# Performance work log

Hardware: AMD Instinct MI355X
Metric: run time of the kernel (lower is better)

The kernel has to match this reference:

```python
import jax, jax.numpy as jnp
import numpy as np

NUM_HEADS = 16


def setup_inputs() -> dict:
    key = jax.random.key(0)
    ks = jax.random.split(key, 6)
    B, N, L, C = 2, 1024, 4096, 1024
    x_obj = jax.random.normal(ks[0], (B, N, C), dtype=jnp.float32)
    x_ctx = jax.random.normal(ks[1], (B, L, C), dtype=jnp.float32)
    s = 1.0 / np.sqrt(C)
    Wq = jax.random.normal(ks[2], (C, C), dtype=jnp.float32) * s
    Wkv = jax.random.normal(ks[3], (C, 2 * C), dtype=jnp.float32) * s
    Wproj = jax.random.normal(ks[4], (C, C), dtype=jnp.float32) * s
    bproj = jax.random.normal(ks[5], (C,), dtype=jnp.float32) * 0.01
    return {"x_obj": x_obj, "x_ctx": x_ctx, "Wq": Wq, "Wkv": Wkv,
            "Wproj": Wproj, "bproj": bproj}


def _split_heads(t, H):
    # [B, T, C] -> [B, H, T, d]
    B, T, C = t.shape
    return t.reshape(B, T, H, C // H).transpose(0, 2, 1, 3)


def reference(x_obj, x_ctx, Wq, Wkv, Wproj, bproj):
    B, N, C = x_obj.shape
    H = NUM_HEADS
    d = C // H
    scale = d ** -0.5

    q = _split_heads(x_obj @ Wq, H)                      # [B,H,N,d]

    kv_o = x_obj @ Wkv                                   # [B,N,2C] -> (2,H,d) split
    k_obj = _split_heads(kv_o[..., :C], H)               # [B,H,N,d]
    v_obj = _split_heads(kv_o[..., C:], H)

    kv_c = x_ctx @ Wkv                                   # [B,L,2C]
    k_ctx = _split_heads(kv_c[..., :C], H)               # [B,H,L,d]
    v_ctx = _split_heads(kv_c[..., C:], H)

    k = jnp.concatenate([k_obj, k_ctx], axis=2)          # [B,H,N+L,d]
    v = jnp.concatenate([v_obj, v_ctx], axis=2)

    attn = jnp.einsum('bhnd,bhmd->bhnm', q, k) * scale   # [B,H,N,N+L]
    attn = jax.nn.softmax(attn, axis=-1)
    out = jnp.einsum('bhnm,bhmd->bhnd', attn, v)         # [B,H,N,d]
    out = out.transpose(0, 2, 1, 3).reshape(B, N, C)
    return out @ Wproj + bproj
```

## Files before the change

kernel.cpp:

```cpp
#include <hip/hip_runtime.h>
#include <stdint.h>

typedef unsigned short u16;
typedef unsigned int   u32;
typedef __attribute__((ext_vector_type(8))) short bf16x8;
typedef __attribute__((ext_vector_type(4))) float f32x4;

__device__ __forceinline__ u16 f2bf(float f) {
    union { float f; u32 u; } v; v.f = f;
    return (u16)((v.u + 0x7FFFu + ((v.u >> 16) & 1u)) >> 16);
}
__device__ __forceinline__ float bf2f(u16 h) {
    union { u32 u; float f; } v; v.u = ((u32)h) << 16; return v.f;
}

__device__ __forceinline__ void async16(const u16* g, u16* l) {
    typedef __attribute__((address_space(1))) const u32 gq;
    typedef __attribute__((address_space(3))) u32 lq;
    __builtin_amdgcn_global_load_lds((gq*)g, (lq*)l, 16, 0, 0);
}

__global__ void cvt_cat_k(const float* __restrict__ xo, const float* __restrict__ xc,
                          u16* __restrict__ Xc)
{
    int t = blockIdx.x * 256 + threadIdx.x;
    int row = t >> 8, cid = (t & 255) * 4;
    int b = row >= 5120, s = row - b * 5120;
    const float* src = (s < 1024)
        ? xo + ((size_t)(b * 1024 + s)) * 1024 + cid
        : xc + ((size_t)(b * 4096 + s - 1024)) * 1024 + cid;
    float4 f = *(const float4*)src;
    union { u16 a[4]; uint2 v; } p;
    p.a[0] = f2bf(f.x); p.a[1] = f2bf(f.y); p.a[2] = f2bf(f.z); p.a[3] = f2bf(f.w);
    *(uint2*)(Xc + (size_t)row * 1024 + cid) = p.v;
}

__global__ void cvt_w_k(const float* __restrict__ Wq, const float* __restrict__ Wkv,
                        const float* __restrict__ Wp,
                        u16* __restrict__ Wqt, u16* __restrict__ Wkt,
                        u16* __restrict__ Wpt)
{
    __shared__ __align__(16) u16 Ts[64][72];
    int id = blockIdx.x;
    const float* W; u16* Wt; int N, tile;
    if (id < 256)      { W = Wq;  Wt = Wqt; N = 1024; tile = id; }
    else if (id < 768) { W = Wkv; Wt = Wkt; N = 2048; tile = id - 256; }
    else               { W = Wp;  Wt = Wpt; N = 1024; tile = id - 768; }
    int nt = N >> 6;
    int n0 = (tile % nt) * 64, k0 = (tile / nt) * 64;

    int t = threadIdx.x;
    int lr = t >> 2, lc = (t & 3) * 16;
    const float* src = W + (size_t)(k0 + lr) * N + n0 + lc;
    union { u16 a[8]; uint4 v; } p0, p1;
    float4 f0 = *(const float4*)(src),      f1 = *(const float4*)(src + 4);
    float4 f2 = *(const float4*)(src + 8),  f3 = *(const float4*)(src + 12);
    p0.a[0]=f2bf(f0.x); p0.a[1]=f2bf(f0.y); p0.a[2]=f2bf(f0.z); p0.a[3]=f2bf(f0.w);
    p0.a[4]=f2bf(f1.x); p0.a[5]=f2bf(f1.y); p0.a[6]=f2bf(f1.z); p0.a[7]=f2bf(f1.w);
    p1.a[0]=f2bf(f2.x); p1.a[1]=f2bf(f2.y); p1.a[2]=f2bf(f2.z); p1.a[3]=f2bf(f2.w);
    p1.a[4]=f2bf(f3.x); p1.a[5]=f2bf(f3.y); p1.a[6]=f2bf(f3.z); p1.a[7]=f2bf(f3.w);
    *(uint4*)&Ts[lr][lc]     = p0.v;
    *(uint4*)&Ts[lr][lc + 8] = p1.v;
    __syncthreads();
    union { u16 a[8]; uint4 v; } q0, q1;
#pragma unroll
    for (int j = 0; j < 8; ++j) q0.a[j] = Ts[lc + j][lr];
#pragma unroll
    for (int j = 0; j < 8; ++j) q1.a[j] = Ts[lc + 8 + j][lr];
    u16* dst = Wt + (size_t)(n0 + lr) * 1024 + k0 + lc;
    *(uint4*)dst       = q0.v;
    *(uint4*)(dst + 8) = q1.v;
}

__global__ __launch_bounds__(256, 2)
void gemm_qkv(const u16* __restrict__ A, const u16* __restrict__ Wqt,
              const u16* __restrict__ Wkt, u16* __restrict__ q,
              u16* __restrict__ Kh, u16* __restrict__ Vh)
{
    __shared__ __align__(16) u16 smem[17408];
    u16* As = smem;
    u16* Bs = smem + 4096;

    const int t = threadIdx.x, w = t >> 6;
    const int lane = t & 63, quad = lane >> 4, l16 = lane & 15;
    const int id = blockIdx.x;
    const bool qm = id >= 1280;
    int m0, n0; const u16* Bt;
    if (qm) { int t2 = id - 1280; m0 = (t2 >> 3) * 128; n0 = (t2 & 7) * 128; Bt = Wqt; }
    else    { m0 = (id >> 4) * 128; n0 = (id & 15) * 128; Bt = Wkt; }
    const int wr = (w >> 1) * 64, wc = (w & 1) * 64;

    const int sr0 = w * 32 + (lane >> 2), sr1 = sr0 + 16;
    const int cg  = (lane & 3) ^ ((lane >> 4) & 3);
    u16* abase = As + w * 1024;
    u16* bbase = Bs + w * 1024;

    const u16 *ar0, *ar1;
    {
        int g0 = m0 + sr0, g1 = m0 + sr1;
        if (qm) {
            ar0 = A + ((size_t)(g0 >> 10) * 5120 + (g0 & 1023)) * 1024;
            ar1 = A + ((size_t)(g1 >> 10) * 5120 + (g1 & 1023)) * 1024;
        } else {
            ar0 = A + (size_t)g0 * 1024;
            ar1 = A + (size_t)g1 * 1024;
        }
        ar0 += cg * 8; ar1 += cg * 8;
    }
    const u16* br0 = Bt + (size_t)(n0 + sr0) * 1024 + cg * 8;
    const u16* br1 = Bt + (size_t)(n0 + sr1) * 1024 + cg * 8;

    f32x4 acc[4][4] = {};
    const int sel = (quad ^ (l16 >> 2)) * 8;

    for (int k0 = 0; k0 < 1024; k0 += 32) {
        async16(ar0 + k0, abase);
        async16(ar1 + k0, abase + 512);
        async16(br0 + k0, bbase);
        async16(br1 + k0, bbase + 512);
        __syncthreads();

        bf16x8 av[4], bv[4];
#pragma unroll
        for (int i = 0; i < 4; ++i)
            av[i] = *(const bf16x8*)&As[(wr + i * 16 + l16) * 32 + sel];
#pragma unroll
        for (int j = 0; j < 4; ++j)
            bv[j] = *(const bf16x8*)&Bs[(wc + j * 16 + l16) * 32 + sel];
#pragma unroll
        for (int i = 0; i < 4; ++i)
#pragma unroll
            for (int j = 0; j < 4; ++j)
                acc[i][j] = __builtin_amdgcn_mfma_f32_16x16x32_bf16(av[i], bv[j], acc[i][j], 0, 0, 0);
        __syncthreads();
    }

    if (qm) {
#pragma unroll
        for (int j = 0; j < 4; ++j) {
            int col = n0 + wc + j * 16 + l16;
#pragma unroll
            for (int i = 0; i < 4; ++i) {
                int rowb = m0 + wr + i * 16 + quad * 4;
#pragma unroll
                for (int r = 0; r < 4; ++r)
                    q[(size_t)(rowb + r) * 1024 + col] = f2bf(acc[i][j][r]);
            }
        }
    } else if (n0 < 1024) {
#pragma unroll
        for (int j = 0; j < 4; ++j) {
            int col = n0 + wc + j * 16 + l16;
#pragma unroll
            for (int i = 0; i < 4; ++i) {
                int rowb = m0 + wr + i * 16 + quad * 4;
                int b = rowb >= 5120;
                int key = rowb - b * 5120;
                int bh = b * 16 + (col >> 6), d = col & 63;
                u16* dst = Kh + ((size_t)bh * 5120 + key) * 64 + d;
#pragma unroll
                for (int r = 0; r < 4; ++r) dst[r * 64] = f2bf(acc[i][j][r]);
            }
        }
    } else {
        u16* Tv = smem;
#pragma unroll
        for (int j = 0; j < 4; ++j) {
            int d2 = wc + j * 16 + l16;
#pragma unroll
            for (int i = 0; i < 4; ++i) {
                int kl = wr + i * 16 + quad * 4;
                union { u16 a[4]; uint2 v; } pk;
#pragma unroll
                for (int r = 0; r < 4; ++r) pk.a[r] = f2bf(acc[i][j][r]);
                *(uint2*)&Tv[d2 * 136 + kl] = pk.v;
            }
        }
        __syncthreads();
        int b = m0 >= 5120;
        int keyb = m0 - b * 5120;
        int hb = (n0 - 1024) >> 6;
#pragma unroll
        for (int p = 0; p < 8; ++p) {
            int idx = p * 256 + t;
            int d2 = idx >> 4, k0c = (idx & 15) * 8;
            uint4 vv = *(const uint4*)&Tv[d2 * 136 + k0c];
            int bh = b * 16 + hb + (d2 >> 6), d = d2 & 63;
            *(uint4*)(Vh + ((size_t)bh * 64 + d) * 5120 + keyb + k0c) = vv;
        }
    }
}

__global__ __launch_bounds__(256, 2)
void gemm_proj(const u16* __restrict__ A, const u16* __restrict__ Bt,
               const float* __restrict__ bias, float* __restrict__ Cf)
{
    __shared__ __align__(16) u16 As[128 * 32];
    __shared__ __align__(16) u16 Bs[64 * 32];

    const int t = threadIdx.x, w = t >> 6;
    const int lane = t & 63, quad = lane >> 4, l16 = lane & 15;
    const int m0 = blockIdx.y * 128, n0 = blockIdx.x * 64;
    const int wr = w * 32, wc = 0;

    const int sr0 = w * 32 + (lane >> 2), sr1 = sr0 + 16;
    const int cg  = (lane & 3) ^ ((lane >> 4) & 3);
    u16* abase = As + w * 1024;
    u16* bbase = Bs + w * 512;

    const u16* ar0 = A + (size_t)(m0 + sr0) * 1024 + cg * 8;
    const u16* ar1 = A + (size_t)(m0 + sr1) * 1024 + cg * 8;
    const u16* br0 = Bt + (size_t)(n0 + w * 16 + (lane >> 2)) * 1024 + cg * 8;

    f32x4 acc[2][4] = {};
    const int sel = (quad ^ (l16 >> 2)) * 8;

    for (int k0 = 0; k0 < 1024; k0 += 32) {
        async16(ar0 + k0, abase);
        async16(ar1 + k0, abase + 512);
        async16(br0 + k0, bbase);
        __syncthreads();

        bf16x8 av[2], bv[4];
#pragma unroll
        for (int i = 0; i < 2; ++i)
            av[i] = *(const bf16x8*)&As[(wr + i * 16 + l16) * 32 + sel];
#pragma unroll
        for (int j = 0; j < 4; ++j)
            bv[j] = *(const bf16x8*)&Bs[(wc + j * 16 + l16) * 32 + sel];
#pragma unroll
        for (int i = 0; i < 2; ++i)
#pragma unroll
            for (int j = 0; j < 4; ++j)
                acc[i][j] = __builtin_amdgcn_mfma_f32_16x16x32_bf16(av[i], bv[j], acc[i][j], 0, 0, 0);
        __syncthreads();
    }

#pragma unroll
    for (int j = 0; j < 4; ++j) {
        int col = n0 + wc + j * 16 + l16;
        float bvl = bias[col];
#pragma unroll
        for (int i = 0; i < 2; ++i) {
            int rowb = m0 + wr + i * 16 + quad * 4;
#pragma unroll
            for (int r = 0; r < 4; ++r)
                Cf[(size_t)(rowb + r) * 1024 + col] = acc[i][j][r] + bvl;
        }
    }
}

__global__ __launch_bounds__(256, 4)
void attn_k(const u16* __restrict__ Q, const u16* __restrict__ Kh,
            const u16* __restrict__ Vh, u16* __restrict__ Op,
            float* __restrict__ Lp)
{
    __shared__ __align__(16) u16 Ks[64][72];
    __shared__ __align__(16) u16 Vt[64][72];
    __shared__ __align__(16) u16 Ps[4][32][72];

    const int tid  = threadIdx.x;
    const int wave = tid >> 6, lane = tid & 63;
    const int quad = lane >> 4, l16 = lane & 15;
    const int bx = blockIdx.x;
    const int part = bx & 3, qt = (bx >> 2) & 7, h = (bx >> 5) & 15, b = bx >> 9;
    const int bh = b * 16 + h;

    const int qrow0 = b * 1024 + qt * 128 + wave * 32;
    const u16* qbase = Q + (size_t)qrow0 * 1024 + h * 64;

    bf16x8 aq[2][2];
#pragma unroll
    for (int rt = 0; rt < 2; ++rt) {
        aq[rt][0] = *(const bf16x8*)(qbase + (size_t)(rt * 16 + l16) * 1024 +      quad * 8);
        aq[rt][1] = *(const bf16x8*)(qbase + (size_t)(rt * 16 + l16) * 1024 + 32 + quad * 8);
    }

    f32x4 o[2][4] = {};
    f32x4 lv[2] = {};

    const u16* kbase = Kh + (size_t)bh * 5120 * 64;
    const u16* vbase = Vh + (size_t)bh * 64 * 5120;
    const int skey = tid >> 2, sdc = (tid & 3) * 16;
    const int m_beg = part * 1280;

    for (int c = 0; c < 20; ++c) {
        const int m0 = m_beg + c * 64;
        {
            const u16* src = kbase + (size_t)(m0 + skey) * 64 + sdc;
            *(uint4*)&Ks[skey][sdc]     = *(const uint4*)(src);
            *(uint4*)&Ks[skey][sdc + 8] = *(const uint4*)(src + 8);
        }
        {
            const u16* vsrc = vbase + (size_t)skey * 5120 + m0 + sdc;
            *(uint4*)&Vt[skey][sdc]     = *(const uint4*)(vsrc);
            *(uint4*)&Vt[skey][sdc + 8] = *(const uint4*)(vsrc + 8);
        }
        __syncthreads();

        f32x4 s[2][4] = {};
#pragma unroll
        for (int nt = 0; nt < 4; ++nt) {
            bf16x8 kb0 = *(const bf16x8*)&Ks[nt * 16 + l16][     quad * 8];
            bf16x8 kb1 = *(const bf16x8*)&Ks[nt * 16 + l16][32 + quad * 8];
#pragma unroll
            for (int rt = 0; rt < 2; ++rt) {
                s[rt][nt] = __builtin_amdgcn_mfma_f32_16x16x32_bf16(aq[rt][0], kb0, s[rt][nt], 0, 0, 0);
                s[rt][nt] = __builtin_amdgcn_mfma_f32_16x16x32_bf16(aq[rt][1], kb1, s[rt][nt], 0, 0, 0);
            }
        }

#pragma unroll
        for (int rt = 0; rt < 2; ++rt)
#pragma unroll
            for (int nt = 0; nt < 4; ++nt)
#pragma unroll
                for (int r = 0; r < 4; ++r) {
                    float e = __expf(s[rt][nt][r] * 0.125f);
                    lv[rt][r] += e;
                    Ps[wave][rt * 16 + quad * 4 + r][nt * 16 + l16] = f2bf(e);
                }

        asm volatile("s_waitcnt lgkmcnt(0)" ::: "memory");

        bf16x8 pf[2][2];
#pragma unroll
        for (int rt = 0; rt < 2; ++rt) {
            pf[rt][0] = *(const bf16x8*)&Ps[wave][rt * 16 + l16][     quad * 8];
            pf[rt][1] = *(const bf16x8*)&Ps[wave][rt * 16 + l16][32 + quad * 8];
        }

#pragma unroll
        for (int dt = 0; dt < 4; ++dt) {
            bf16x8 v0 = *(const bf16x8*)&Vt[dt * 16 + l16][     quad * 8];
            bf16x8 v1 = *(const bf16x8*)&Vt[dt * 16 + l16][32 + quad * 8];
#pragma unroll
            for (int rt = 0; rt < 2; ++rt) {
                o[rt][dt] = __builtin_amdgcn_mfma_f32_16x16x32_bf16(pf[rt][0], v0, o[rt][dt], 0, 0, 0);
                o[rt][dt] = __builtin_amdgcn_mfma_f32_16x16x32_bf16(pf[rt][1], v1, o[rt][dt], 0, 0, 0);
            }
        }
        __syncthreads();
    }

    float lsum[2][4];
#pragma unroll
    for (int rt = 0; rt < 2; ++rt)
#pragma unroll
        for (int r = 0; r < 4; ++r) {
            float x = lv[rt][r];
#pragma unroll
            for (int off = 8; off >= 1; off >>= 1)
                x += __shfl_xor(x, off, 64);
            lsum[rt][r] = x;
        }

    const int Rb = bh * 1024 + qt * 128 + wave * 32;
    u16* obase = Op + ((size_t)part << 21);
#pragma unroll
    for (int rt = 0; rt < 2; ++rt)
#pragma unroll
        for (int dt = 0; dt < 4; ++dt)
#pragma unroll
            for (int r = 0; r < 4; ++r) {
                int R = Rb + rt * 16 + quad * 4 + r;
                obase[(size_t)R * 64 + dt * 16 + l16] = f2bf(o[rt][dt][r]);
            }
    if (l16 == 0) {
#pragma unroll
        for (int rt = 0; rt < 2; ++rt)
#pragma unroll
            for (int r = 0; r < 4; ++r)
                Lp[part * 32768 + Rb + rt * 16 + quad * 4 + r] = lsum[rt][r];
    }
}

__global__ void comb_k(const u16* __restrict__ Op, const float* __restrict__ Lp,
                       u16* __restrict__ ao)
{
    int t = blockIdx.x * 256 + threadIdx.x;
    int R = t >> 4, dg = (t & 15) * 4;
    float l = Lp[R] + Lp[32768 + R] + Lp[65536 + R] + Lp[98304 + R];
    float a[4] = {0.f, 0.f, 0.f, 0.f};
#pragma unroll
    for (int p = 0; p < 4; ++p) {
        union { u16 a[4]; uint2 v; } w;
        w.v = *(const uint2*)(Op + ((size_t)p << 21) + (size_t)R * 64 + dg);
#pragma unroll
        for (int j = 0; j < 4; ++j) a[j] += bf2f(w.a[j]);
    }
    float inv = 1.f / l;
    int bh = R >> 10, n = R & 1023, b = bh >> 4, h = bh & 15;
    union { u16 a[4]; uint2 v; } out;
#pragma unroll
    for (int j = 0; j < 4; ++j) out.a[j] = f2bf(a[j] * inv);
    *(uint2*)(ao + (size_t)(b * 1024 + n) * 1024 + h * 64 + dg) = out.v;
}

extern "C" void kernel_launch(void* const* d_in, const int* in_sizes, int n_in,
                              void* d_out, int out_size, void* d_ws, size_t ws_size,
                              hipStream_t stream)
{
    const float* x_obj = (const float*)d_in[0];
    const float* x_ctx = (const float*)d_in[1];
    const float* Wq    = (const float*)d_in[2];
    const float* Wkv   = (const float*)d_in[3];
    const float* Wproj = (const float*)d_in[4];
    const float* bproj = (const float*)d_in[5];
    float* out = (float*)d_out;

    u16* Xc  = (u16*)d_ws;
    u16* ao  = Xc;
    u16* Op  = Xc + (size_t)2097152;
    u16* Wqt = Xc  + (size_t)10485760;
    u16* Wkt = Wqt + (size_t)1048576;
    u16* Wpt = Wkt + (size_t)2097152;
    u16* q   = Wpt + (size_t)1048576;
    u16* Kh  = q   + (size_t)2097152;
    u16* Vh  = Kh  + (size_t)10485760;
    float* Lp = (float*)(Vh + (size_t)10485760);

    dim3 blk(256);
    cvt_cat_k<<<dim3(10240), blk, 0, stream>>>(x_obj, x_ctx, Xc);
    cvt_w_k<<<dim3(1024), blk, 0, stream>>>(Wq, Wkv, Wproj, Wqt, Wkt, Wpt);

    gemm_qkv<<<dim3(1408), blk, 0, stream>>>(Xc, Wqt, Wkt, q, Kh, Vh);
    attn_k<<<dim3(1024), blk, 0, stream>>>(q, Kh, Vh, Op, Lp);
    comb_k<<<dim3(2048), blk, 0, stream>>>(Op, Lp, ao);
    gemm_proj<<<dim3(16, 16), blk, 0, stream>>>(ao, Wpt, bproj, out);
}
```

Before: 255.7 us.

## Swizzle attention LDS tiles, repack V on load, merge conversion kernels

```diff
diff --git a/kernel.cpp b/kernel.cpp
--- a/kernel.cpp
+++ b/kernel.cpp
@@ -13,6 +13,9 @@
 __device__ __forceinline__ float bf2f(u16 h) {
     union { u32 u; float f; } v; v.u = ((u32)h) << 16; return v.f;
 }
+__device__ __forceinline__ u32 fbits(float f) {
+    union { float f; u32 u; } v; v.f = f; return v.u;
+}
 
 __device__ __forceinline__ void async16(const u16* g, u16* l) {
     typedef __attribute__((address_space(1))) const u32 gq;
@@ -20,36 +23,34 @@
     __builtin_amdgcn_global_load_lds((gq*)g, (lq*)l, 16, 0, 0);
 }
 
-__global__ void cvt_cat_k(const float* __restrict__ xo, const float* __restrict__ xc,
-                          u16* __restrict__ Xc)
-{
-    int t = blockIdx.x * 256 + threadIdx.x;
-    int row = t >> 8, cid = (t & 255) * 4;
-    int b = row >= 5120, s = row - b * 5120;
-    const float* src = (s < 1024)
-        ? xo + ((size_t)(b * 1024 + s)) * 1024 + cid
-        : xc + ((size_t)(b * 4096 + s - 1024)) * 1024 + cid;
-    float4 f = *(const float4*)src;
-    union { u16 a[4]; uint2 v; } p;
-    p.a[0] = f2bf(f.x); p.a[1] = f2bf(f.y); p.a[2] = f2bf(f.z); p.a[3] = f2bf(f.w);
-    *(uint2*)(Xc + (size_t)row * 1024 + cid) = p.v;
-}
-
-__global__ void cvt_w_k(const float* __restrict__ Wq, const float* __restrict__ Wkv,
-                        const float* __restrict__ Wp,
-                        u16* __restrict__ Wqt, u16* __restrict__ Wkt,
-                        u16* __restrict__ Wpt)
+__global__ void cvt_all_k(const float* __restrict__ xo, const float* __restrict__ xc,
+                          u16* __restrict__ Xc,
+                          const float* __restrict__ Wq, const float* __restrict__ Wkv,
+                          const float* __restrict__ Wp,
+                          u16* __restrict__ Wqt, u16* __restrict__ Wkt,
+                          u16* __restrict__ Wpt)
 {
     __shared__ __align__(16) u16 Ts[64][72];
-    int id = blockIdx.x;
+    int id = blockIdx.x, t = threadIdx.x;
+    if (id < 10240) {
+        int row = id, cid = t * 4;
+        int b = row >= 5120, s = row - b * 5120;
+        const float* src = (s < 1024)
+            ? xo + ((size_t)(b * 1024 + s)) * 1024 + cid
+            : xc + ((size_t)(b * 4096 + s - 1024)) * 1024 + cid;
+        float4 f = *(const float4*)src;
+        union { u16 a[4]; uint2 v; } p;
+        p.a[0]=f2bf(f.x); p.a[1]=f2bf(f.y); p.a[2]=f2bf(f.z); p.a[3]=f2bf(f.w);
+        *(uint2*)(Xc + (size_t)row * 1024 + cid) = p.v;
+        return;
+    }
+    int wid = id - 10240;
     const float* W; u16* Wt; int N, tile;
-    if (id < 256)      { W = Wq;  Wt = Wqt; N = 1024; tile = id; }
-    else if (id < 768) { W = Wkv; Wt = Wkt; N = 2048; tile = id - 256; }
-    else               { W = Wp;  Wt = Wpt; N = 1024; tile = id - 768; }
+    if (wid < 256)      { W = Wq;  Wt = Wqt; N = 1024; tile = wid; }
+    else if (wid < 768) { W = Wkv; Wt = Wkt; N = 2048; tile = wid - 256; }
+    else                { W = Wp;  Wt = Wpt; N = 1024; tile = wid - 768; }
     int nt = N >> 6;
     int n0 = (tile % nt) * 64, k0 = (tile / nt) * 64;
-
-    int t = threadIdx.x;
     int lr = t >> 2, lc = (t & 3) * 16;
     const float* src = W + (size_t)(k0 + lr) * N + n0 + lc;
     union { u16 a[8]; uint4 v; } p0, p1;
@@ -72,7 +73,7 @@
     *(uint4*)(dst + 8) = q1.v;
 }
 
-__global__ __launch_bounds__(256, 2)
+__global__ __launch_bounds__(256, 3)
 void gemm_qkv(const u16* __restrict__ A, const u16* __restrict__ Wqt,
               const u16* __restrict__ Wkt, u16* __restrict__ q,
               u16* __restrict__ Kh, u16* __restrict__ Vh)
@@ -201,7 +202,7 @@
     const int t = threadIdx.x, w = t >> 6;
     const int lane = t & 63, quad = lane >> 4, l16 = lane & 15;
     const int m0 = blockIdx.y * 128, n0 = blockIdx.x * 64;
-    const int wr = w * 32, wc = 0;
+    const int wr = w * 32;
 
     const int sr0 = w * 32 + (lane >> 2), sr1 = sr0 + 16;
     const int cg  = (lane & 3) ^ ((lane >> 4) & 3);
@@ -227,7 +228,7 @@
             av[i] = *(const bf16x8*)&As[(wr + i * 16 + l16) * 32 + sel];
 #pragma unroll
         for (int j = 0; j < 4; ++j)
-            bv[j] = *(const bf16x8*)&Bs[(wc + j * 16 + l16) * 32 + sel];
+            bv[j] = *(const bf16x8*)&Bs[(j * 16 + l16) * 32 + sel];
 #pragma unroll
         for (int i = 0; i < 2; ++i)
 #pragma unroll
@@ -238,7 +239,7 @@
 
 #pragma unroll
     for (int j = 0; j < 4; ++j) {
-        int col = n0 + wc + j * 16 + l16;
+        int col = n0 + j * 16 + l16;
         float bvl = bias[col];
 #pragma unroll
         for (int i = 0; i < 2; ++i) {
@@ -255,9 +256,9 @@
             const u16* __restrict__ Vh, u16* __restrict__ Op,
             float* __restrict__ Lp)
 {
-    __shared__ __align__(16) u16 Ks[64][72];
-    __shared__ __align__(16) u16 Vt[64][72];
-    __shared__ __align__(16) u16 Ps[4][32][72];
+    __shared__ __align__(16) u16 Ks[4096];
+    __shared__ __align__(16) u16 Vt[4096];
+    __shared__ __align__(16) u16 Ps[8192];
 
     const int tid  = threadIdx.x;
     const int wave = tid >> 6, lane = tid & 63;
@@ -281,28 +282,51 @@
 
     const u16* kbase = Kh + (size_t)bh * 5120 * 64;
     const u16* vbase = Vh + (size_t)bh * 64 * 5120;
-    const int skey = tid >> 2, sdc = (tid & 3) * 16;
+    const int srow = tid >> 2;
+    const int scg  = (tid & 3) * 2;
+    const int m7   = srow & 7;
+    const int l7   = l16 & 7;
+    u16* kdst0 = Ks + srow * 64 + ((scg ^ m7) * 8);
+    u16* kdst1 = Ks + srow * 64 + (((scg + 1) ^ m7) * 8);
+    u16* vdst0 = Vt + srow * 64 + ((scg ^ m7) * 8);
+    u16* vdst1 = Vt + srow * 64 + (((scg + 1) ^ m7) * 8);
+    u16* psw   = Ps + wave * 2048;
     const int m_beg = part * 1280;
+    const float SC = 0.180336880f;
 
     for (int c = 0; c < 20; ++c) {
         const int m0 = m_beg + c * 64;
         {
-            const u16* src = kbase + (size_t)(m0 + skey) * 64 + sdc;
-            *(uint4*)&Ks[skey][sdc]     = *(const uint4*)(src);
-            *(uint4*)&Ks[skey][sdc + 8] = *(const uint4*)(src + 8);
+            const u16* ks = kbase + (size_t)(m0 + srow) * 64 + scg * 8;
+            *(uint4*)kdst0 = *(const uint4*)(ks);
+            *(uint4*)kdst1 = *(const uint4*)(ks + 8);
         }
         {
-            const u16* vsrc = vbase + (size_t)skey * 5120 + m0 + sdc;
-            *(uint4*)&Vt[skey][sdc]     = *(const uint4*)(vsrc);
-            *(uint4*)&Vt[skey][sdc + 8] = *(const uint4*)(vsrc + 8);
+            const u16* vs = vbase + (size_t)srow * 5120 + m0 + (tid & 3) * 4;
+            uint2 g0 = *(const uint2*)(vs);
+            uint2 g1 = *(const uint2*)(vs + 16);
+            uint2 g2 = *(const uint2*)(vs + 32);
+            uint2 g3 = *(const uint2*)(vs + 48);
+            uint4 o0, o1;
+            o0.x = __builtin_amdgcn_perm(g1.x, g0.x, 0x05040100u);
+            o0.y = __builtin_amdgcn_perm(g3.x, g2.x, 0x05040100u);
+            o0.z = __builtin_amdgcn_perm(g1.x, g0.x, 0x07060302u);
+            o0.w = __builtin_amdgcn_perm(g3.x, g2.x, 0x07060302u);
+            o1.x = __builtin_amdgcn_perm(g1.y, g0.y, 0x05040100u);
+            o1.y = __builtin_amdgcn_perm(g3.y, g2.y, 0x05040100u);
+            o1.z = __builtin_amdgcn_perm(g1.y, g0.y, 0x07060302u);
+            o1.w = __builtin_amdgcn_perm(g3.y, g2.y, 0x07060302u);
+            *(uint4*)vdst0 = o0;
+            *(uint4*)vdst1 = o1;
         }
         __syncthreads();
 
         f32x4 s[2][4] = {};
 #pragma unroll
         for (int nt = 0; nt < 4; ++nt) {
-            bf16x8 kb0 = *(const bf16x8*)&Ks[nt * 16 + l16][     quad * 8];
-            bf16x8 kb1 = *(const bf16x8*)&Ks[nt * 16 + l16][32 + quad * 8];
+            const u16* krow = Ks + (nt * 16 + l16) * 64;
+            bf16x8 kb0 = *(const bf16x8*)(krow + ((quad     ^ l7) * 8));
+            bf16x8 kb1 = *(const bf16x8*)(krow + (((4+quad) ^ l7) * 8));
 #pragma unroll
             for (int rt = 0; rt < 2; ++rt) {
                 s[rt][nt] = __builtin_amdgcn_mfma_f32_16x16x32_bf16(aq[rt][0], kb0, s[rt][nt], 0, 0, 0);
@@ -313,27 +337,35 @@
 #pragma unroll
         for (int rt = 0; rt < 2; ++rt)
 #pragma unroll
-            for (int nt = 0; nt < 4; ++nt)
-#pragma unroll
-                for (int r = 0; r < 4; ++r) {
-                    float e = __expf(s[rt][nt][r] * 0.125f);
-                    lv[rt][r] += e;
-                    Ps[wave][rt * 16 + quad * 4 + r][nt * 16 + l16] = f2bf(e);
-                }
+            for (int r = 0; r < 4; ++r) {
+                float e0 = exp2f(s[rt][0][r] * SC);
+                float e1 = exp2f(s[rt][1][r] * SC);
+                float e2 = exp2f(s[rt][2][r] * SC);
+                float e3 = exp2f(s[rt][3][r] * SC);
+                lv[rt][r] += (e0 + e1) + (e2 + e3);
+                uint2 pw;
+                pw.x = __builtin_amdgcn_perm(fbits(e1), fbits(e0), 0x07060302u);
+                pw.y = __builtin_amdgcn_perm(fbits(e3), fbits(e2), 0x07060302u);
+                int qr = quad * 4 + r;
+                *(uint2*)(psw + (rt * 16 + qr) * 64 +
+                          (((l16 >> 1) ^ (qr & 7)) * 8) + (l16 & 1) * 4) = pw;
+            }
 
         asm volatile("s_waitcnt lgkmcnt(0)" ::: "memory");
 
         bf16x8 pf[2][2];
 #pragma unroll
         for (int rt = 0; rt < 2; ++rt) {
-            pf[rt][0] = *(const bf16x8*)&Ps[wave][rt * 16 + l16][     quad * 8];
-            pf[rt][1] = *(const bf16x8*)&Ps[wave][rt * 16 + l16][32 + quad * 8];
+            const u16* prow = psw + (rt * 16 + l16) * 64;
+            pf[rt][0] = *(const bf16x8*)(prow + ((quad     ^ l7) * 8));
+            pf[rt][1] = *(const bf16x8*)(prow + (((4+quad) ^ l7) * 8));
         }
 
 #pragma unroll
         for (int dt = 0; dt < 4; ++dt) {
-            bf16x8 v0 = *(const bf16x8*)&Vt[dt * 16 + l16][     quad * 8];
-            bf16x8 v1 = *(const bf16x8*)&Vt[dt * 16 + l16][32 + quad * 8];
+            const u16* vrow = Vt + (dt * 16 + l16) * 64;
+            bf16x8 v0 = *(const bf16x8*)(vrow + ((quad     ^ l7) * 8));
+            bf16x8 v1 = *(const bf16x8*)(vrow + (((4+quad) ^ l7) * 8));
 #pragma unroll
             for (int rt = 0; rt < 2; ++rt) {
                 o[rt][dt] = __builtin_amdgcn_mfma_f32_16x16x32_bf16(pf[rt][0], v0, o[rt][dt], 0, 0, 0);
@@ -421,9 +453,8 @@
     float* Lp = (float*)(Vh + (size_t)10485760);
 
     dim3 blk(256);
-    cvt_cat_k<<<dim3(10240), blk, 0, stream>>>(x_obj, x_ctx, Xc);
-    cvt_w_k<<<dim3(1024), blk, 0, stream>>>(Wq, Wkv, Wproj, Wqt, Wkt, Wpt);
-
+    cvt_all_k<<<dim3(11264), blk, 0, stream>>>(x_obj, x_ctx, Xc,
+                                               Wq, Wkv, Wproj, Wqt, Wkt, Wpt);
     gemm_qkv<<<dim3(1408), blk, 0, stream>>>(Xc, Wqt, Wkt, q, Kh, Vh);
     attn_k<<<dim3(1024), blk, 0, stream>>>(q, Kh, Vh, Op, Lp);
     comb_k<<<dim3(2048), blk, 0, stream>>>(Op, Lp, ao);
```

New measurement: 261.6 us. 2.3% more time.
